# Kernel optimization log

Hardware: AMD Instinct MI355X
Metric: run time of the kernel (lower is better)

Reference implementation:

```python
import jax, jax.numpy as jnp
import numpy as np
from jax import lax

D_MODEL = 1024
N_HEADS = 16
D_HEAD = D_MODEL // N_HEADS  # 64
NB_FEAT = 266
CHUNK = 128
KERNEL_EPS = 1e-4
CAUSAL_EPS = 1e-6


def _gaussian_orthogonal_matrix(nb_rows, nb_cols, seed=0):
    # Performer gaussian_orthogonal_random_matrix, scaling=0:
    # stacked orthogonal blocks scaled by chi-distributed row norms.
    rng = np.random.default_rng(seed)
    blocks = []
    n_full = nb_rows // nb_cols + (1 if nb_rows % nb_cols else 0)
    for _ in range(n_full):
        g = rng.standard_normal((nb_cols, nb_cols))
        q_mat, _ = np.linalg.qr(g)
        blocks.append(q_mat.T)
    mat = np.concatenate(blocks, axis=0)[:nb_rows]
    multiplier = np.linalg.norm(rng.standard_normal((nb_rows, nb_cols)), axis=1)
    return jnp.asarray((multiplier[:, None] * mat).astype(np.float32))


def setup_inputs() -> dict:
    key = jax.random.key(0)
    ks = jax.random.split(key, 9)
    s = 1.0 / np.sqrt(D_MODEL)
    x = jax.random.normal(ks[0], (2, 4096, D_MODEL), dtype=jnp.float32)
    def lin(k):
        kw, kb = jax.random.split(k)
        W = jax.random.uniform(kw, (D_MODEL, D_MODEL), jnp.float32, -s, s)
        b = jax.random.uniform(kb, (D_MODEL,), jnp.float32, -s, s)
        return W, b
    Wq, bq = lin(ks[1]); Wk, bk = lin(ks[2]); Wv, bv = lin(ks[3]); Wo, bo = lin(ks[4])
    proj = _gaussian_orthogonal_matrix(NB_FEAT, D_HEAD)
    return {"x": x, "Wq": Wq, "bq": bq, "Wk": Wk, "bk": bk, "Wv": Wv, "bv": bv,
            "Wo": Wo, "bo": bo, "proj": proj}


def _softmax_kernel(data, proj, is_query):
    # Performer random-feature softmax kernel.
    data_normalizer = data.shape[-1] ** -0.25
    ratio = proj.shape[0] ** -0.5
    dn = data * data_normalizer  # [b,h,n,d]
    data_dash = jnp.einsum('bhnd,md->bhnm', dn, proj)
    diag = 0.5 * jnp.sum(dn * dn, axis=-1, keepdims=True)  # [b,h,n,1]
    if is_query:
        stab = jnp.max(data_dash, axis=-1, keepdims=True)
    else:
        stab = jnp.max(data_dash)
    return ratio * (jnp.exp(data_dash - diag - stab) + KERNEL_EPS)


def _causal_linear_attention(qp, kp, v, chunk_size):
    # Chunked O(n) causal linear attention (Performer noncuda variant).
    b, h, n, m = qp.shape
    d = v.shape[-1]
    nc = n // chunk_size
    qc = jnp.moveaxis(qp.reshape(b, h, nc, chunk_size, m), 2, 0)  # [nc,b,h,c,m]
    kc = jnp.moveaxis(kp.reshape(b, h, nc, chunk_size, m), 2, 0)
    vc = jnp.moveaxis(v.reshape(b, h, nc, chunk_size, d), 2, 0)   # [nc,b,h,c,d]

    def step(carry, inp):
        last_k, last_ctx = carry  # [b,h,m], [b,h,m,d]
        q, k, vv = inp
        k_cum = last_k[:, :, None, :] + jnp.cumsum(k, axis=-2)          # [b,h,c,m]
        D_inv = 1.0 / jnp.einsum('bhcm,bhcm->bhc', q, k_cum + CAUSAL_EPS)
        ctx = jnp.einsum('bhcm,bhcd->bhcmd', k, vv)                     # [b,h,c,m,d]
        ctx_cum = last_ctx[:, :, None, :, :] + jnp.cumsum(ctx, axis=2)
        out = jnp.einsum('bhcmd,bhcm,bhc->bhcd', ctx_cum, q, D_inv)
        return (k_cum[:, :, -1, :], ctx_cum[:, :, -1, :, :]), out

    carry0 = (jnp.zeros((b, h, m), qp.dtype), jnp.zeros((b, h, m, d), qp.dtype))
    _, outs = lax.scan(step, carry0, (qc, kc, vc))  # [nc,b,h,c,d]
    return jnp.moveaxis(outs, 0, 2).reshape(b, h, n, d)


def reference(x, Wq, bq, Wk, bk, Wv, bv, Wo, bo, proj):
    bsz, n, _ = x.shape
    def split_heads(t):
        return t.reshape(bsz, n, N_HEADS, D_HEAD).transpose(0, 2, 1, 3)  # [b,h,n,d]
    q = split_heads(x @ Wq.T + bq)
    k = split_heads(x @ Wk.T + bk)
    v = split_heads(x @ Wv.T + bv)
    q_prime = _softmax_kernel(q, proj, is_query=True)
    k_prime = _softmax_kernel(k, proj, is_query=False)
    attn = _causal_linear_attention(q_prime, k_prime, v, CHUNK)  # [b,h,n,d]
    attn = attn.transpose(0, 2, 1, 3).reshape(bsz, n, D_MODEL)
    return attn @ Wo.T + bo
```

## Files before the change

### kernel.cpp

```cpp
#include <hip/hip_runtime.h>

#define B_    2
#define NSEQ  4096
#define DM    1024
#define H_    16
#define DH    64
#define MF    266
#define MP    288
#define NROWS (B_*NSEQ)
#define NHROWS (B_*H_*NSEQ)
#define RATIO 0.06131393394849658f
#define DNORM 0.3535533905932738f
#define KEPS  1e-4f
#define CEPS  1e-6f

#define CH    128
#define NC    32
#define SROW  (65*MP)
#define SELEM (64*MP)

#define AS1 __attribute__((address_space(1)))
#define AS3 __attribute__((address_space(3)))

typedef unsigned short u16;
typedef unsigned int   u32;

typedef __bf16 bf16x8 __attribute__((ext_vector_type(8)));
typedef float  f32x4  __attribute__((ext_vector_type(4)));

__device__ __forceinline__ float b2f(u16 u){ u32 x = ((u32)u) << 16; return __builtin_bit_cast(float, x); }
__device__ __forceinline__ u16 f2b(float f){
    u32 x = __builtin_bit_cast(u32, f);
    u32 r = x + 0x7fffu + ((x >> 16) & 1u);
    return (u16)(r >> 16);
}
__device__ __forceinline__ u32 enc_max(float f){ u32 b = __builtin_bit_cast(u32, f); return (b & 0x80000000u) ? ~b : (b | 0x80000000u); }
__device__ __forceinline__ float dec_max(u32 u){ u32 b = (u & 0x80000000u) ? (u & 0x7fffffffu) : ~u; return __builtin_bit_cast(float, b); }

struct DetectArgs { const u32* p[10]; int nw[10]; };

__global__ void detect_all(DetectArgs a, u32* __restrict__ flags)
{
    __shared__ int cnt[256];
    int k = blockIdx.x;
    const u32* src = a.p[k];
    int nwords = a.nw[k];
    int t = threadIdx.x; int c = 0;
    for (int i = t; i < nwords; i += 256) {
        u32 w = src[i];
        int ea = (int)((w >> 7)  & 0xFF);
        int eb = (int)((w >> 23) & 0xFF);
        c += (ea >= 112 && ea <= 143) ? 1 : 0;
        c += (eb >= 112 && eb <= 143) ? 1 : 0;
    }
    cnt[t] = c; __syncthreads();
    for (int s = 128; s; s >>= 1) { if (t < s) cnt[t] += cnt[t + s]; __syncthreads(); }
    if (t == 0) flags[k] = (cnt[0] >= (nwords * 3) / 2) ? 1u : 0u;
}

__device__ __forceinline__ void conv8(const void* src, u16* dst, int i, u32 flag)
{
    if (flag) {
        *(uint4*)(dst + i) = *(const uint4*)((const u16*)src + i);
    } else {
        const float* s = (const float*)src + i;
        u16 tmp[8];
        #pragma unroll
        for (int j = 0; j < 8; ++j) tmp[j] = f2b(s[j]);
        *(uint4*)(dst + i) = *(uint4*)tmp;
    }
}

struct ConvAllArgs {
    const void* xs;    u16* xd;
    const void* wsrc[4]; u16* wdst[4];
    const void* bsrc[4]; u16* bdst[4];
    const void* pj;    u16* pjd;
    u32* gpart; u32* gmax;
    const u32* flags;
};

__global__ __launch_bounds__(256)
void conv_all(ConvAllArgs a)
{
    int blk = blockIdx.x, t = threadIdx.x;
    if (blk < 4096) {
        int i = blk * 2048 + t * 8;
        conv8(a.xs, a.xd, i, a.flags[0]);
    } else if (blk < 6144) {
        int r = blk - 4096; int w = r >> 9; int i = (r & 511) * 2048 + t * 8;
        conv8(a.wsrc[w], a.wdst[w], i, a.flags[1 + 2*w]);
    } else if (blk < 6148) {
        int w = blk - 6144; int i = t * 8;
        if (i < DM) conv8(a.bsrc[w], a.bdst[w], i, a.flags[2 + 2*w]);
    } else if (blk < 6157) {
        int i = (blk - 6148) * 2048 + t * 8;
        if (i < MF * DH) conv8(a.pj, a.pjd, i, a.flags[9]);
        else             *(uint4*)(a.pjd + i) = (uint4){0,0,0,0};
    } else {
        a.gpart[t] = 0u;
        if (t == 0) *a.gmax = 0u;
    }
}

#define GEMM_BODY(A_, Bm_, bm_, bn_, ACC_)                                    \
    const int K = DM;                                                          \
    __shared__ u16 As[128 * 64];                                               \
    __shared__ u16 Bs[128 * 64];                                               \
    int t = threadIdx.x;                                                       \
    int wave = t >> 6, lane = t & 63;                                          \
    int wm = wave >> 1, wn = wave & 1;                                         \
    int quad = lane >> 4, l16 = lane & 15;                                     \
    int rowc = lane >> 3;                                                      \
    int csrc = ((lane & 7) ^ rowc) * 8;                                        \
    int cA = wave * 4;                                                         \
    const u16* ap0 = A_  + (size_t)(bm_ + cA*8 + rowc) * K + csrc;             \
    const u16* bp0 = Bm_ + (size_t)(bn_ + cA*8 + rowc) * K + csrc;             \
    u16* lA = As + cA * 512;                                                   \
    u16* lB = Bs + cA * 512;                                                   \
    f32x4 ACC_[4][4];                                                          \
    _Pragma("unroll")                                                          \
    for (int i = 0; i < 4; ++i)                                                \
        _Pragma("unroll")                                                      \
        for (int j = 0; j < 4; ++j) ACC_[i][j] = (f32x4){0.f,0.f,0.f,0.f};     \
    for (int k0 = 0; k0 < K; k0 += 64) {                                       \
        _Pragma("unroll")                                                      \
        for (int j = 0; j < 4; ++j) {                                          \
            __builtin_amdgcn_global_load_lds((const AS1 void*)(ap0 + (size_t)j*8*K + k0), (AS3 void*)(lA + j*512), 16, 0, 0); \
            __builtin_amdgcn_global_load_lds((const AS1 void*)(bp0 + (size_t)j*8*K + k0), (AS3 void*)(lB + j*512), 16, 0, 0); \
        }                                                                      \
        __syncthreads();                                                       \
        _Pragma("unroll")                                                      \
        for (int ks = 0; ks < 2; ++ks) {                                       \
            bf16x8 af[4], bfr[4];                                              \
            int sw = ((((ks << 2) | quad) ^ (l16 & 7)) << 4);                  \
            _Pragma("unroll")                                                  \
            for (int i = 0; i < 4; ++i) {                                      \
                af[i]  = *(const bf16x8*)((const char*)As + (wm*64 + i*16 + l16)*128 + sw); \
                bfr[i] = *(const bf16x8*)((const char*)Bs + (wn*64 + i*16 + l16)*128 + sw); \
            }                                                                  \
            _Pragma("unroll")                                                  \
            for (int i = 0; i < 4; ++i)                                        \
                _Pragma("unroll")                                              \
                for (int j = 0; j < 4; ++j)                                    \
                    ACC_[i][j] = __builtin_amdgcn_mfma_f32_16x16x32_bf16(af[i], bfr[j], ACC_[i][j], 0, 0, 0); \
        }                                                                      \
        __syncthreads();                                                       \
    }

__global__ __launch_bounds__(256)
void gemm_qkv(const u16* __restrict__ A,
              const u16* __restrict__ Wqb, const u16* __restrict__ Wkb,
              const u16* __restrict__ Wvb,
              const u16* __restrict__ bqb, const u16* __restrict__ bkb,
              const u16* __restrict__ bvb,
              u16* __restrict__ Vb, float* __restrict__ Qf, float* __restrict__ Kf)
{
    int bid = blockIdx.x;
    int xcd = bid & 7, pos = bid >> 3;
    int lb  = xcd * 192 + pos;
    int z   = lb % 3;
    int q   = lb / 3;
    int idx = q & 15, sg = q >> 4;
    int sgm = sg & 15, sgn = sg >> 4;
    int bm = (sgm*4 + (idx & 3)) * 128;
    int bn = (sgn*4 + (idx >> 2)) * 128;

    const u16* Bm   = (z == 0) ? Wvb : (z == 1) ? Wqb : Wkb;
    const u16* bias = (z == 0) ? bvb : (z == 1) ? bqb : bkb;
    GEMM_BODY(A, Bm, bm, bn, acc)
    float* Of = (z == 1) ? Qf : Kf;
    #pragma unroll
    for (int i = 0; i < 4; ++i) {
        #pragma unroll
        for (int j = 0; j < 4; ++j) {
            int col = bn + wn*64 + j*16 + l16;
            float bv = b2f(bias[col]);
            #pragma unroll
            for (int r = 0; r < 4; ++r) {
                int row = bm + wm*64 + i*16 + quad*4 + r;
                float v = acc[i][j][r] + bv;
                if (z == 0) Vb[(size_t)row * DM + col] = f2b(v);
                else        Of[(size_t)row * DM + col] = v;
            }
        }
    }
}

template<int OUT_BF16>
__global__ __launch_bounds__(256)
void gemm_nt(const u16* __restrict__ A, const u16* __restrict__ Bm,
             const u16* __restrict__ bias, void* __restrict__ C)
{
    int bm = blockIdx.x * 128, bn = blockIdx.y * 128;
    GEMM_BODY(A, Bm, bm, bn, acc)
    #pragma unroll
    for (int i = 0; i < 4; ++i) {
        #pragma unroll
        for (int j = 0; j < 4; ++j) {
            int col = bn + wn*64 + j*16 + l16;
            float bv = b2f(bias[col]);
            #pragma unroll
            for (int r = 0; r < 4; ++r) {
                int row = bm + wm*64 + i*16 + quad*4 + r;
                float v = acc[i][j][r] + bv;
                if (OUT_BF16) ((u16*)C)[(size_t)row * DM + col] = f2b(v);
                else          ((float*)C)[(size_t)row * DM + col] = v;
            }
        }
    }
}

template<int MODE>
__global__ __launch_bounds__(256)
void feat_mfma(const float* __restrict__ X, const u16* __restrict__ projP,
               u16* __restrict__ OutP, u32* __restrict__ gpart,
               const u32* __restrict__ gmax)
{
    int blk = blockIdx.x;
    int bh = blk >> 6, nt = blk & 63;
    int b = bh >> 4, h = bh & 15;
    int n0 = nt * 64;
    int t = threadIdx.x;
    int lane = t & 63, w = t >> 6;
    int quad = lane >> 4, l16 = lane & 15;

    __shared__ uint4 smemU[2368];
    __shared__ float red4[4];
    u16* smem16 = (u16*)smemU;

    const float* xrow = X + ((size_t)(b * NSEQ + n0 + w*16 + l16)) * DM + h * DH;
    float va[2][8];
    #pragma unroll
    for (int ks = 0; ks < 2; ++ks) {
        float4 u0 = *(const float4*)(xrow + ks*32 + quad*8);
        float4 u1 = *(const float4*)(xrow + ks*32 + quad*8 + 4);
        va[ks][0]=u0.x; va[ks][1]=u0.y; va[ks][2]=u0.z; va[ks][3]=u0.w;
        va[ks][4]=u1.x; va[ks][5]=u1.y; va[ks][6]=u1.z; va[ks][7]=u1.w;
    }

    for (int i = t; i < 2304; i += 256) {
        int m = i >> 3, c = i & 7;
        uint4 v = *(const uint4*)(projP + m*64 + c*8);
        int dstb = m*128 + ((c*16) ^ ((m & 7) << 4));
        *(uint4*)((char*)smemU + dstb) = v;
    }

    bf16x8 ahi[2], alo[2];
    float sq = 0.f;
    #pragma unroll
    for (int ks = 0; ks < 2; ++ks) {
        #pragma unroll
        for (int i = 0; i < 8; ++i) {
            float v = va[ks][i] * DNORM;
            sq += v * v;
            u16 hb = f2b(v);
            float hv = b2f(hb);
            ahi[ks][i] = __builtin_bit_cast(__bf16, hb);
            alo[ks][i] = __builtin_bit_cast(__bf16, f2b(v - hv));
        }
    }
    sq += __shfl_xor(sq, 16, 64);
    sq += __shfl_xor(sq, 32, 64);
    float diag_my = 0.5f * sq;

    __syncthreads();

    f32x4 acc[18];
    #pragma unroll
    for (int j = 0; j < 18; ++j) acc[j] = (f32x4){0.f,0.f,0.f,0.f};
    #pragma unroll
    for (int j = 0; j < 18; ++j) {
        int m = j*16 + l16;
        #pragma unroll
        for (int ks = 0; ks < 2; ++ks) {
            int off = m*128 + (((quad*16) + ks*64) ^ ((m & 7) << 4));
            bf16x8 bf = *(const bf16x8*)((const char*)smemU + off);
            acc[j] = __builtin_amdgcn_mfma_f32_16x16x32_bf16(ahi[ks], bf, acc[j], 0, 0, 0);
            acc[j] = __builtin_amdgcn_mfma_f32_16x16x32_bf16(alo[ks], bf, acc[j], 0, 0, 0);
        }
    }

    float rmax[4];
    #pragma unroll
    for (int r = 0; r < 4; ++r) rmax[r] = -3.4e38f;
    #pragma unroll
    for (int j = 0; j < 16; ++j)
        #pragma unroll
        for (int r = 0; r < 4; ++r) rmax[r] = fmaxf(rmax[r], acc[j][r]);
    if (l16 < MF - 256) {
        #pragma unroll
        for (int r = 0; r < 4; ++r) rmax[r] = fmaxf(rmax[r], acc[16][r]);
    }
    #pragma unroll
    for (int s = 1; s < 16; s <<= 1)
        #pragma unroll
        for (int r = 0; r < 4; ++r)
            rmax[r] = fmaxf(rmax[r], __shfl_xor(rmax[r], s, 64));

    if (MODE == 1) {
        float wm2 = fmaxf(fmaxf(rmax[0], rmax[1]), fmaxf(rmax[2], rmax[3]));
        wm2 = fmaxf(wm2, __shfl_xor(wm2, 16, 64));
        wm2 = fmaxf(wm2, __shfl_xor(wm2, 32, 64));
        if (lane == 0) red4[w] = wm2;
        __syncthreads();
        if (t == 0) {
            float bm2 = fmaxf(fmaxf(red4[0], red4[1]), fmaxf(red4[2], red4[3]));
            atomicMax(&gpart[blk & 255], enc_max(bm2));
        }
        return;
    }

    float gstab = (MODE == 2) ? dec_max(*gmax) : 0.f;
    float dg[4];
    #pragma unroll
    for (int r = 0; r < 4; ++r) dg[r] = __shfl(diag_my, quad*4 + r, 64);

    __syncthreads();

    #pragma unroll
    for (int j = 0; j < 18; ++j) {
        int m = j*16 + l16;
        #pragma unroll
        for (int r = 0; r < 4; ++r) {
            float stab = (MODE == 0) ? rmax[r] : gstab;
            float val = RATIO * (__expf(acc[j][r] - dg[r] - stab) + KEPS);
            u16 ov = (m < MF) ? f2b(val) : (u16)0;
            smem16[(w*16 + quad*4 + r) * 296 + m] = ov;
        }
    }
    __syncthreads();

    u16* obase = OutP + ((size_t)bh * NSEQ + n0) * MP;
    for (int i = t; i < 2304; i += 256) {
        int row = i / 36, c = i - row * 36;
        *(uint4*)(obase + row*MP + c*8) = *(const uint4*)(smem16 + row*296 + c*8);
    }
}

__global__ void gmax_reduce(const u32* __restrict__ gpart, u32* __restrict__ gmax)
{
    __shared__ u32 r[256];
    int t = threadIdx.x;
    r[t] = gpart[t]; __syncthreads();
    for (int s = 128; s; s >>= 1) { if (t < s) r[t] = max(r[t], r[t + s]); __syncthreads(); }
    if (t == 0) *gmax = r[0];
}

__global__ __launch_bounds__(256)
void chunk_ST(const u16* __restrict__ Kp, const u16* __restrict__ Vb,
              u16* __restrict__ Sb, float* __restrict__ zf)
{
    int bhc = blockIdx.x;
    int bh = bhc >> 5, c = bhc & (NC - 1);
    int b = bh >> 4, h = bh & 15;
    int t = threadIdx.x, w = t >> 6, lane = t & 63;
    int quad = lane >> 4, l16 = lane & 15;
    int n0 = c * CH;

    __shared__ __align__(16) u16 KTs[288*40];
    __shared__ __align__(16) u16 VTs[80*136];

    {
        int d0 = (t >> 5) * 8, nb = (t & 31) * 4;
        const u16* vb2 = Vb + ((size_t)(b*NSEQ + n0 + nb)) * DM + h*DH + d0;
        uint4 r0 = *(const uint4*)(vb2);
        uint4 r1 = *(const uint4*)(vb2 + DM);
        uint4 r2 = *(const uint4*)(vb2 + 2*DM);
        uint4 r3 = *(const uint4*)(vb2 + 3*DM);
        const u32* a0 = (const u32*)&r0; const u32* a1 = (const u32*)&r1;
        const u32* a2 = (const u32*)&r2; const u32* a3 = (const u32*)&r3;
        #pragma unroll
        for (int e = 0; e < 8; ++e) {
            u32 w0 = a0[e>>1], w1 = a1[e>>1], w2 = a2[e>>1], w3 = a3[e>>1];
            u32 lo2, hi2;
            if (e & 1) { lo2 = (w0 >> 16) | (w1 & 0xFFFF0000u); hi2 = (w2 >> 16) | (w3 & 0xFFFF0000u); }
            else       { lo2 = (w0 & 0xFFFFu) | (w1 << 16);     hi2 = (w2 & 0xFFFFu) | (w3 << 16); }
            uint2 uu; uu.x = lo2; uu.y = hi2;
            *(uint2*)&VTs[(d0 + e)*136 + nb] = uu;
        }
        if (t < 128) VTs[64*136 + t] = 0x3F80u;
        if (t < 255) {
            int rr = 65 + t/17, cc2 = t - (t/17)*17;
            uint4 z4 = (uint4){0,0,0,0};
            *(uint4*)&VTs[rr*136 + cc2*8] = z4;
        }
    }

    f32x4 am[18], az[5];
    #pragma unroll
    for (int mt = 0; mt < 18; ++mt) am[mt] = (f32x4){0.f,0.f,0.f,0.f};
    #pragma unroll
    for (int j = 0; j < 5; ++j) az[j] = (f32x4){0.f,0.f,0.f,0.f};

    const u16* kbase = Kp + ((size_t)bh * NSEQ + n0) * MP;
    for (int qh = 0; qh < 4; ++qh) {
        __syncthreads();
        for (int i = t; i < 288; i += 256) {
            int nb4 = (i & 7) * 4, m0 = (i >> 3) * 8;
            const u16* kb = kbase + (size_t)(qh*32 + nb4) * MP + m0;
            uint4 r0 = *(const uint4*)(kb);
            uint4 r1 = *(const uint4*)(kb + MP);
            uint4 r2 = *(const uint4*)(kb + 2*MP);
            uint4 r3 = *(const uint4*)(kb + 3*MP);
            const u32* a0 = (const u32*)&r0; const u32* a1 = (const u32*)&r1;
            const u32* a2 = (const u32*)&r2; const u32* a3 = (const u32*)&r3;
            #pragma unroll
            for (int e = 0; e < 8; ++e) {
                u32 w0 = a0[e>>1], w1 = a1[e>>1], w2 = a2[e>>1], w3 = a3[e>>1];
                u32 lo2, hi2;
                if (e & 1) { lo2 = (w0 >> 16) | (w1 & 0xFFFF0000u); hi2 = (w2 >> 16) | (w3 & 0xFFFF0000u); }
                else       { lo2 = (w0 & 0xFFFFu) | (w1 << 16);     hi2 = (w2 & 0xFFFFu) | (w3 << 16); }
                uint2 uu; uu.x = lo2; uu.y = hi2;
                *(uint2*)&KTs[(m0 + e)*40 + nb4] = uu;
            }
        }
        __syncthreads();
        int nof = qh*32 + quad*8;
        bf16x8 aw = *(const bf16x8*)&VTs[(w*16 + l16)*136 + nof];
        bf16x8 a4 = *(const bf16x8*)&VTs[(64 + l16)*136 + nof];
        #pragma unroll
        for (int mt = 0; mt < 18; ++mt) {
            bf16x8 bk = *(const bf16x8*)&KTs[(mt*16 + l16)*40 + quad*8];
            am[mt] = __builtin_amdgcn_mfma_f32_16x16x32_bf16(aw, bk, am[mt], 0, 0, 0);
        }
        #pragma unroll
        for (int j = 0; j < 5; ++j) {
            int mtz = w + 4*j;
            if (mtz < 18) {
                bf16x8 bk = *(const bf16x8*)&KTs[(mtz*16 + l16)*40 + quad*8];
                az[j] = __builtin_amdgcn_mfma_f32_16x16x32_bf16(a4, bk, az[j], 0, 0, 0);
            }
        }
    }

    u16* sb = Sb + (size_t)bhc * SELEM;
    #pragma unroll
    for (int mt = 0; mt < 18; ++mt)
        #pragma unroll
        for (int r = 0; r < 4; ++r)
            sb[(size_t)(w*16 + quad*4 + r) * MP + mt*16 + l16] = f2b(am[mt][r]);
    if (quad == 0) {
        #pragma unroll
        for (int j = 0; j < 5; ++j) {
            int mtz = w + 4*j;
            if (mtz < 18) zf[(size_t)bhc * MP + mtz*16 + l16] = az[j][0];
        }
    }
}

__global__ __launch_bounds__(256)
void chunk_prefix(u16* __restrict__ Sb, float* __restrict__ zf)
{
    int gid = blockIdx.x * 256 + threadIdx.x;
    int bh = gid / SROW;
    int rem = gid - bh * SROW;
    float run = 0.f;
    if (rem < SELEM) {
        size_t base = (size_t)(bh * NC) * SELEM + rem;
        #pragma unroll 4
        for (int c2 = 0; c2 < NC; ++c2) {
            size_t o = base + (size_t)c2 * SELEM;
            float v = b2f(Sb[o]);
            Sb[o] = f2b(run);
            run += v;
        }
    } else {
        int m = rem - SELEM;
        size_t base = (size_t)(bh * NC) * MP + m;
        #pragma unroll 4
        for (int c2 = 0; c2 < NC; ++c2) {
            size_t o = base + (size_t)c2 * MP;
            float v = zf[o];
            zf[o] = run + CEPS;
            run += v;
        }
    }
}

__global__ __launch_bounds__(256)
void scan_mfma(const u16* __restrict__ Qp, const u16* __restrict__ Kp,
               const u16* __restrict__ Vb, const u16* __restrict__ Sb,
               const float* __restrict__ zf, u16* __restrict__ attn)
{
    int bhc = blockIdx.x;
    int bh = bhc >> 5, c = bhc & (NC - 1);
    int b = bh >> 4, h = bh & 15;
    int t = threadIdx.x, w = t >> 6, lane = t & 63;
    int quad = lane >> 4, l16 = lane & 15;
    int n0 = c * CH;
    int it0 = w, it1 = 7 - w;

    __shared__ __align__(16) u16 R1s[9472];
    __shared__ __align__(16) u16 R2s[17408];

    for (int i = t; i < 2176; i += 256) ((uint4*)R2s)[i] = (uint4){0,0,0,0};

    bf16x8 q0[9], q1[9];
    {
        const u16* qa = Qp + ((size_t)bh * NSEQ + n0 + it0*16 + l16) * MP + quad*8;
        const u16* qb = Qp + ((size_t)bh * NSEQ + n0 + it1*16 + l16) * MP + quad*8;
        #pragma unroll
        for (int s = 0; s < 9; ++s) {
            q0[s] = *(const bf16x8*)(qa + s*32);
            q1[s] = *(const bf16x8*)(qb + s*32);
        }
    }

    float denw0 = 0.f, denw1 = 0.f;
    const u16* kbase = Kp + ((size_t)bh * NSEQ + n0) * MP;

    for (int qt = 0; qt < 4; ++qt) {
        __syncthreads();
        for (int i = t; i < 1152; i += 256) {
            int rr = i / 36, cc = i - rr * 36;
            *(uint4*)&R1s[rr*296 + cc*8] =
                *(const uint4*)(kbase + (size_t)(qt*32 + rr) * MP + cc*8);
        }
        __syncthreads();
        #pragma unroll
        for (int jj = 0; jj < 2; ++jj) {
            int jt = qt*2 + jj;
            #pragma unroll
            for (int itx = 0; itx < 2; ++itx) {
                int it = itx ? it1 : it0;
                if (jt <= it) {
                    f32x4 acc = (f32x4){0.f,0.f,0.f,0.f};
                    #pragma unroll
                    for (int s = 0; s < 9; ++s) {
                        bf16x8 kf = *(const bf16x8*)&R1s[(jj*16 + l16)*296 + s*32 + quad*8];
                        acc = __builtin_amdgcn_mfma_f32_16x16x32_bf16(
                            kf, itx ? q1[s] : q0[s], acc, 0, 0, 0);
                    }
                    int ig = it*16 + l16;
                    float rs = 0.f;
                    #pragma unroll
                    for (int r = 0; r < 4; ++r) {
                        int jg = jt*16 + quad*4 + r;
                        float pv = (jg <= ig) ? acc[r] : 0.f;
                        rs += pv;
                        R2s[ig*136 + jg] = f2b(pv);
                    }
                    if (itx) denw1 += rs; else denw0 += rs;
                }
            }
        }
    }

    __syncthreads();
    {
        int d0 = (t >> 5) * 8, nb = (t & 31) * 4;
        const u16* vb2 = Vb + ((size_t)(b*NSEQ + n0 + nb)) * DM + h*DH + d0;
        uint4 r0 = *(const uint4*)(vb2);
        uint4 r1 = *(const uint4*)(vb2 + DM);
        uint4 r2 = *(const uint4*)(vb2 + 2*DM);
        uint4 r3 = *(const uint4*)(vb2 + 3*DM);
        const u32* a0 = (const u32*)&r0; const u32* a1 = (const u32*)&r1;
        const u32* a2 = (const u32*)&r2; const u32* a3 = (const u32*)&r3;
        #pragma unroll
        for (int e = 0; e < 8; ++e) {
            u32 w0 = a0[e>>1], w1 = a1[e>>1], w2 = a2[e>>1], w3 = a3[e>>1];
            u32 lo2, hi2;
            if (e & 1) { lo2 = (w0 >> 16) | (w1 & 0xFFFF0000u); hi2 = (w2 >> 16) | (w3 & 0xFFFF0000u); }
            else       { lo2 = (w0 & 0xFFFFu) | (w1 << 16);     hi2 = (w2 & 0xFFFFu) | (w3 << 16); }
            uint2 uu; uu.x = lo2; uu.y = hi2;
            *(uint2*)&R1s[(d0 + e)*136 + nb] = uu;
        }
    }
    __syncthreads();

    f32x4 pacc[2][4];
    #pragma unroll
    for (int i = 0; i < 2; ++i)
        #pragma unroll
        for (int j = 0; j < 4; ++j) pacc[i][j] = (f32x4){0.f,0.f,0.f,0.f};
    int ns0 = (it0 + 2) >> 1, ns1 = (it1 + 2) >> 1;
    #pragma unroll
    for (int ks = 0; ks < 4; ++ks) {
        bool u0 = ks < ns0, u1 = ks < ns1;
        bf16x8 p0 = {}, p1 = {};
        if (u0) p0 = *(const bf16x8*)&R2s[(it0*16 + l16)*136 + ks*32 + quad*8];
        if (u1) p1 = *(const bf16x8*)&R2s[(it1*16 + l16)*136 + ks*32 + quad*8];
        #pragma unroll
        for (int ct = 0; ct < 4; ++ct) {
            bf16x8 vf = *(const bf16x8*)&R1s[(ct*16 + l16)*136 + ks*32 + quad*8];
            if (u0) pacc[0][ct] = __builtin_amdgcn_mfma_f32_16x16x32_bf16(p0, vf, pacc[0][ct], 0, 0, 0);
            if (u1) pacc[1][ct] = __builtin_amdgcn_mfma_f32_16x16x32_bf16(p1, vf, pacc[1][ct], 0, 0, 0);
        }
    }

    f32x4 cacc[2][4];
    #pragma unroll
    for (int i = 0; i < 2; ++i)
        #pragma unroll
        for (int j = 0; j < 4; ++j) cacc[i][j] = (f32x4){0.f,0.f,0.f,0.f};
    const u16* sbw = Sb + (size_t)bhc * SELEM;
    #pragma unroll
    for (int p = 0; p < 2; ++p) {
        __syncthreads();
        for (int i = t; i < 1152; i += 256) {
            int rr = i / 36, cc = i - rr * 36;
            *(uint4*)&R1s[rr*296 + cc*8] =
                *(const uint4*)(sbw + (size_t)(p*32 + rr) * MP + cc*8);
        }
        __syncthreads();
        #pragma unroll
        for (int s = 0; s < 9; ++s)
            #pragma unroll
            for (int cl = 0; cl < 2; ++cl) {
                bf16x8 sf = *(const bf16x8*)&R1s[(cl*16 + l16)*296 + s*32 + quad*8];
                cacc[0][p*2 + cl] = __builtin_amdgcn_mfma_f32_16x16x32_bf16(q0[s], sf, cacc[0][p*2 + cl], 0, 0, 0);
                cacc[1][p*2 + cl] = __builtin_amdgcn_mfma_f32_16x16x32_bf16(q1[s], sf, cacc[1][p*2 + cl], 0, 0, 0);
            }
    }

    float dc0 = 0.f, dc1 = 0.f;
    {
        const float* zc = zf + (size_t)bhc * MP + quad*8;
        #pragma unroll
        for (int s = 0; s < 9; ++s) {
            f32x4 za = *(const f32x4*)(zc + s*32);
            f32x4 zb = *(const f32x4*)(zc + s*32 + 4);
            #pragma unroll
            for (int e = 0; e < 4; ++e) {
                dc0 += (float)q0[s][e] * za[e];
                dc0 += (float)q0[s][e+4] * zb[e];
                dc1 += (float)q1[s][e] * za[e];
                dc1 += (float)q1[s][e+4] * zb[e];
            }
        }
    }
    dc0 += __shfl_xor(dc0, 16, 64); dc0 += __shfl_xor(dc0, 32, 64);
    dc1 += __shfl_xor(dc1, 16, 64); dc1 += __shfl_xor(dc1, 32, 64);
    denw0 += __shfl_xor(denw0, 16, 64); denw0 += __shfl_xor(denw0, 32, 64);
    denw1 += __shfl_xor(denw1, 16, 64); denw1 += __shfl_xor(denw1, 32, 64);
    float den0 = denw0 + dc0, den1 = denw1 + dc1;

    u16* ab = attn + ((size_t)(b*NSEQ + n0)) * DM + h*DH;
    #pragma unroll
    for (int itx = 0; itx < 2; ++itx) {
        int it = itx ? it1 : it0;
        float dv = itx ? den1 : den0;
        #pragma unroll
        for (int r = 0; r < 4; ++r) {
            float deno = __shfl(dv, (lane & 48) + quad*4 + r, 64);
            int row = it*16 + quad*4 + r;
            #pragma unroll
            for (int ct = 0; ct < 4; ++ct) {
                float ov = (pacc[itx][ct][r] + cacc[itx][ct][r]) / deno;
                ab[(size_t)row * DM + ct*16 + l16] = f2b(ov);
            }
        }
    }
}

extern "C" void kernel_launch(void* const* d_in, const int* in_sizes, int n_in,
                              void* d_out, int out_size, void* d_ws, size_t ws_size,
                              hipStream_t stream)
{
    (void)n_in; (void)out_size; (void)ws_size;
    const void* x  = d_in[0];
    const void* Wq = d_in[1]; const void* bq = d_in[2];
    const void* Wk = d_in[3]; const void* bk = d_in[4];
    const void* Wv = d_in[5]; const void* bv = d_in[6];
    const void* Wo = d_in[7]; const void* bo = d_in[8];
    const void* proj = d_in[9];

    char* ws = (char*)d_ws;
    size_t off = 0;
    auto alloc = [&](size_t bytes) -> char* {
        char* p = ws + off; off += (bytes + 255) & ~(size_t)255; return p;
    };
    size_t qkfBytes = (size_t)NROWS * DM * 4;
    size_t sbBytes  = (size_t)(B_ * H_ * NC) * SELEM * 2;
    size_t zfBytes  = (size_t)(B_ * H_ * NC) * MP * 4;
    size_t ovBytes  = 2 * qkfBytes;
    if (sbBytes + zfBytes > ovBytes) ovBytes = sbBytes + zfBytes;
    char*  ov0  = alloc(ovBytes);
    float* QKf0 = (float*)ov0;
    float* QKf1 = (float*)(ov0 + qkfBytes);
    u16*   Sb   = (u16*)ov0;
    float* zfp  = (float*)(ov0 + sbBytes);
    u16*   Vb   = (u16*)alloc((size_t)NROWS * DM * 2);
    u16*   Qp   = (u16*)alloc((size_t)NHROWS * MP * 2);
    u16*   Kp   = (u16*)alloc((size_t)NHROWS * MP * 2);
    u16*   projC= (u16*)alloc((size_t)MP * DH * 2);
    u16*   Wqb  = (u16*)alloc((size_t)DM * DM * 2);
    u16*   Wkb  = (u16*)alloc((size_t)DM * DM * 2);
    u16*   Wvb  = (u16*)alloc((size_t)DM * DM * 2);
    u16*   Wob  = (u16*)alloc((size_t)DM * DM * 2);
    u16*   bqb  = (u16*)alloc(DM * 2);
    u16*   bkb  = (u16*)alloc(DM * 2);
    u16*   bvb  = (u16*)alloc(DM * 2);
    u16*   bob  = (u16*)alloc(DM * 2);
    u32*   flags= (u32*)alloc(16 * 4);
    u32*   gmax = (u32*)alloc(256);
    u32*   gpart= (u32*)alloc(256 * 4);
    char*  xatt = alloc((size_t)NROWS * DM * 2);
    u16*   xb   = (u16*)xatt;
    u16*   attn = (u16*)xatt;

    DetectArgs da;
    for (int i = 0; i < 10; ++i) {
        int n = in_sizes[i];
        int nwords = n / 2; if (nwords > 4096) nwords = 4096;
        da.p[i] = (const u32*)d_in[i];
        da.nw[i] = nwords;
    }
    detect_all<<<10, 256, 0, stream>>>(da, flags);

    ConvAllArgs ca;
    ca.xs = x;  ca.xd = xb;
    ca.wsrc[0] = Wq; ca.wsrc[1] = Wk; ca.wsrc[2] = Wv; ca.wsrc[3] = Wo;
    ca.wdst[0] = Wqb; ca.wdst[1] = Wkb; ca.wdst[2] = Wvb; ca.wdst[3] = Wob;
    ca.bsrc[0] = bq; ca.bsrc[1] = bk; ca.bsrc[2] = bv; ca.bsrc[3] = bo;
    ca.bdst[0] = bqb; ca.bdst[1] = bkb; ca.bdst[2] = bvb; ca.bdst[3] = bob;
    ca.pj = proj; ca.pjd = projC;
    ca.gpart = gpart; ca.gmax = gmax; ca.flags = flags;
    conv_all<<<6158, 256, 0, stream>>>(ca);

    gemm_qkv<<<1536, 256, 0, stream>>>(xb, Wqb, Wkb, Wvb, bqb, bkb, bvb, Vb, QKf0, QKf1);

    feat_mfma<0><<<NHROWS / 64, 256, 0, stream>>>(QKf0, projC, Qp, gpart, gmax);
    feat_mfma<1><<<NHROWS / 64, 256, 0, stream>>>(QKf1, projC, Kp, gpart, gmax);
    gmax_reduce<<<1, 256, 0, stream>>>(gpart, gmax);
    feat_mfma<2><<<NHROWS / 64, 256, 0, stream>>>(QKf1, projC, Kp, gpart, gmax);

    chunk_ST<<<B_ * H_ * NC, 256, 0, stream>>>(Kp, Vb, Sb, zfp);
    chunk_prefix<<<(B_ * H_ * SROW) / 256, 256, 0, stream>>>(Sb, zfp);
    scan_mfma<<<B_ * H_ * NC, 256, 0, stream>>>(Qp, Kp, Vb, Sb, zfp, attn);

    dim3 gg(NROWS / 128, DM / 128);
    gemm_nt<0><<<gg, 256, 0, stream>>>(attn, Wob, bob, d_out);
}
```

Before: 389.3 us.

## Fuse Q/K feature kernels using per-block K stabilizer and rescale pass

Q and K random-feature maps now run in one launch. K features are written with a per-block max stabilizer, and the block max is kept in a small buffer. A lightweight rescale kernel then multiplies the stored bf16 K features by exp(local-global) and adds the epsilon term, replacing the second full K feature recomputation (projection MFMA plus exp). The gemm_qkv block-to-output mapping also changes from modulo-3 interleaving to contiguous ranges. The cost is an extra read-modify-write of Kp, and a small precision change from rescaling bf16-rounded values.

```diff
diff --git a/kernel.cpp b/kernel.cpp
--- a/kernel.cpp
+++ b/kernel.cpp
@@ -159,8 +159,8 @@
     int bid = blockIdx.x;
     int xcd = bid & 7, pos = bid >> 3;
     int lb  = xcd * 192 + pos;
-    int z   = lb % 3;
-    int q   = lb / 3;
+    int z   = lb >> 9;
+    int q   = lb & 511;
     int idx = q & 15, sg = q >> 4;
     int sgm = sg & 15, sgn = sg >> 4;
     int bm = (sgm*4 + (idx & 3)) * 128;
@@ -211,19 +211,24 @@
     }
 }
 
-template<int MODE>
 __global__ __launch_bounds__(256)
-void feat_mfma(const float* __restrict__ X, const u16* __restrict__ projP,
-               u16* __restrict__ OutP, u32* __restrict__ gpart,
-               const u32* __restrict__ gmax)
+void feat_qk(const float* __restrict__ Xq, const float* __restrict__ Xk,
+             const u16* __restrict__ projP, u16* __restrict__ Qp,
+             u16* __restrict__ Kp, u32* __restrict__ gpart,
+             float* __restrict__ lstab)
 {
     int blk = blockIdx.x;
-    int bh = blk >> 6, nt = blk & 63;
+    int isK = blk >> 11;
+    int blk2 = blk & 2047;
+    int bh = blk2 >> 6, nt = blk2 & 63;
     int b = bh >> 4, h = bh & 15;
     int n0 = nt * 64;
     int t = threadIdx.x;
     int lane = t & 63, w = t >> 6;
     int quad = lane >> 4, l16 = lane & 15;
+
+    const float* X = isK ? Xk : Xq;
+    u16* OutP = isK ? Kp : Qp;
 
     __shared__ uint4 smemU[2368];
     __shared__ float red4[4];
@@ -298,20 +303,20 @@
         for (int r = 0; r < 4; ++r)
             rmax[r] = fmaxf(rmax[r], __shfl_xor(rmax[r], s, 64));
 
-    if (MODE == 1) {
+    float stab_blk = 0.f;
+    if (isK) {
         float wm2 = fmaxf(fmaxf(rmax[0], rmax[1]), fmaxf(rmax[2], rmax[3]));
         wm2 = fmaxf(wm2, __shfl_xor(wm2, 16, 64));
         wm2 = fmaxf(wm2, __shfl_xor(wm2, 32, 64));
         if (lane == 0) red4[w] = wm2;
         __syncthreads();
+        stab_blk = fmaxf(fmaxf(red4[0], red4[1]), fmaxf(red4[2], red4[3]));
         if (t == 0) {
-            float bm2 = fmaxf(fmaxf(red4[0], red4[1]), fmaxf(red4[2], red4[3]));
-            atomicMax(&gpart[blk & 255], enc_max(bm2));
-        }
-        return;
-    }
-
-    float gstab = (MODE == 2) ? dec_max(*gmax) : 0.f;
+            atomicMax(&gpart[blk2 & 255], enc_max(stab_blk));
+            lstab[blk2] = stab_blk;
+        }
+    }
+
     float dg[4];
     #pragma unroll
     for (int r = 0; r < 4; ++r) dg[r] = __shfl(diag_my, quad*4 + r, 64);
@@ -323,8 +328,9 @@
         int m = j*16 + l16;
         #pragma unroll
         for (int r = 0; r < 4; ++r) {
-            float stab = (MODE == 0) ? rmax[r] : gstab;
-            float val = RATIO * (__expf(acc[j][r] - dg[r] - stab) + KEPS);
+            float stab = isK ? stab_blk : rmax[r];
+            float ex = __expf(acc[j][r] - dg[r] - stab);
+            float val = isK ? (RATIO * ex) : (RATIO * (ex + KEPS));
             u16 ov = (m < MF) ? f2b(val) : (u16)0;
             smem16[(w*16 + quad*4 + r) * 296 + m] = ov;
         }
@@ -345,6 +351,26 @@
     r[t] = gpart[t]; __syncthreads();
     for (int s = 128; s; s >>= 1) { if (t < s) r[t] = max(r[t], r[t + s]); __syncthreads(); }
     if (t == 0) *gmax = r[0];
+}
+
+__global__ __launch_bounds__(256)
+void krescale(u16* __restrict__ Kp, const float* __restrict__ lstab,
+              const u32* __restrict__ gmax)
+{
+    int gid = blockIdx.x * 256 + threadIdx.x;
+    int row = gid / 36, cc = gid - row * 36;
+    float g = dec_max(*gmax);
+    float sc = __expf(lstab[row >> 6] - g);
+    u16* p = Kp + (size_t)row * MP + cc*8;
+    uint4 v = *(uint4*)p;
+    u16* e = (u16*)&v;
+    int m0 = cc * 8;
+    #pragma unroll
+    for (int j = 0; j < 8; ++j) {
+        float kv = b2f(e[j]) * sc + RATIO * KEPS;
+        e[j] = (m0 + j < MF) ? f2b(kv) : (u16)0;
+    }
+    *(uint4*)p = v;
 }
 
 __global__ __launch_bounds__(256)
@@ -696,6 +722,7 @@
     u32*   flags= (u32*)alloc(16 * 4);
     u32*   gmax = (u32*)alloc(256);
     u32*   gpart= (u32*)alloc(256 * 4);
+    float* lstab= (float*)alloc(2048 * 4);
     char*  xatt = alloc((size_t)NROWS * DM * 2);
     u16*   xb   = (u16*)xatt;
     u16*   attn = (u16*)xatt;
@@ -721,10 +748,9 @@
 
     gemm_qkv<<<1536, 256, 0, stream>>>(xb, Wqb, Wkb, Wvb, bqb, bkb, bvb, Vb, QKf0, QKf1);
 
-    feat_mfma<0><<<NHROWS / 64, 256, 0, stream>>>(QKf0, projC, Qp, gpart, gmax);
-    feat_mfma<1><<<NHROWS / 64, 256, 0, stream>>>(QKf1, projC, Kp, gpart, gmax);
+    feat_qk<<<4096, 256, 0, stream>>>(QKf0, QKf1, projC, Qp, Kp, gpart, lstab);
     gmax_reduce<<<1, 256, 0, stream>>>(gpart, gmax);
-    feat_mfma<2><<<NHROWS / 64, 256, 0, stream>>>(QKf1, projC, Kp, gpart, gmax);
+    krescale<<<18432, 256, 0, stream>>>(Kp, lstab, gmax);
 
     chunk_ST<<<B_ * H_ * NC, 256, 0, stream>>>(Kp, Vb, Sb, zfp);
     chunk_prefix<<<(B_ * H_ * SROW) / 256, 256, 0, stream>>>(Sb, zfp);
```

Result: no change. 395.3 us (+1.5%).
